# Performance work log

Hardware: AMD Instinct MI355X
Metric: run time of the kernel (lower is better)

Reference implementation:

```python
import jax, jax.numpy as jnp
import numpy as np

H = 1024        # bridge_hidden_dim
NH = 16         # num_attention_heads
HD = H // NH    # head_dim = 64
B, S = 4, 1024
PHYS_W = 0.2
CONS_W = 0.15


def setup_inputs() -> dict:
    key = jax.random.key(0)
    ks = jax.random.split(key, 16)
    sc = 0.02
    return {
        "cnn_features": jax.random.normal(ks[0], (B, S, H), jnp.float32),
        "llm_features": jax.random.normal(ks[1], (B, S, H), jnp.float32),
        "Wq": jax.random.normal(ks[2], (H, H), jnp.float32) * sc,
        "bq": jnp.zeros((H,), jnp.float32),
        "Wk": jax.random.normal(ks[3], (H, H), jnp.float32) * sc,
        "bk": jnp.zeros((H,), jnp.float32),
        "Wv": jax.random.normal(ks[4], (H, H), jnp.float32) * sc,
        "bv": jnp.zeros((H,), jnp.float32),
        "Wo": jax.random.normal(ks[5], (H, H), jnp.float32) * sc,
        "bo": jnp.zeros((H,), jnp.float32),
        "ln_g": jnp.ones((H,), jnp.float32),
        "ln_b": jnp.zeros((H,), jnp.float32),
        "e_energy": jax.random.normal(ks[6], (H,), jnp.float32),
        "e_mass": jax.random.normal(ks[7], (H,), jnp.float32),
        "e_momentum": jax.random.normal(ks[8], (H,), jnp.float32),
    }


def _layernorm(x, g, b, eps=1e-5):
    mu = jnp.mean(x, axis=-1, keepdims=True)
    var = jnp.var(x, axis=-1, keepdims=True)
    return (x - mu) * jax.lax.rsqrt(var + eps) * g + b


def _split_heads(x):
    b, s, _ = x.shape
    return x.reshape(b, s, NH, HD).transpose(0, 2, 1, 3)  # [b, h, s, d]


def _physics_attention(q_in, k_in, v_in, Wq, bq, Wk, bk, Wv, bv, Wo, bo, ln_g, ln_b):
    # q_in: [b, sq, H]; k_in == v_in: [b, sk, H] with sq == sk (required by bias math)
    Q = _split_heads(q_in @ Wq.T + bq)  # [b,h,s,d]
    K = _split_heads(k_in @ Wk.T + bk)
    V = _split_heads(v_in @ Wv.T + bv)
    scores = jnp.einsum('bhqd,bhkd->bhqk', Q, K) / jnp.sqrt(jnp.float32(HD))
    # physics constraints (broadcast [b,h,s,1] over key axis)
    energy_bias = jnp.sum(Q * K, axis=-1, keepdims=True) * PHYS_W
    mass_bias = jnp.mean(Q + K, axis=-1, keepdims=True) * CONS_W
    scores = scores + energy_bias + mass_bias
    attn = jax.nn.softmax(scores, axis=-1)  # dropout is identity in eval
    att = jnp.einsum('bhqk,bhkd->bhqd', attn, V)
    b, h, s, d = att.shape
    att = att.transpose(0, 2, 1, 3).reshape(b, s, h * d)
    out = att @ Wo.T + bo
    return _layernorm(q_in + out, ln_g, ln_b)


def reference(cnn_features, llm_features, Wq, bq, Wk, bk, Wv, bv, Wo, bo,
              ln_g, ln_b, e_energy, e_mass, e_momentum):
    b = cnn_features.shape[0]
    phys = jnp.stack([e_energy, e_mass, e_momentum], axis=0)  # [3, H]
    phys = jnp.broadcast_to(phys[None], (b, 3, H))
    aug_cnn = jnp.concatenate([cnn_features, phys], axis=1)  # [b, S+3, H]
    aug_llm = jnp.concatenate([llm_features, phys], axis=1)
    cnn_att = _physics_attention(aug_cnn, aug_llm, aug_llm,
                                 Wq, bq, Wk, bk, Wv, bv, Wo, bo, ln_g, ln_b)
    llm_att = _physics_attention(aug_llm, aug_cnn, aug_cnn,
                                 Wq, bq, Wk, bk, Wv, bv, Wo, bo, ln_g, ln_b)
    cnn_out = cnn_att[:, :cnn_features.shape[1], :]
    llm_out = llm_att[:, :llm_features.shape[1], :]
    return (cnn_out, llm_out)
```

## Files before the change

kernel.cpp:

```cpp
#include <hip/hip_runtime.h>
#include <stdint.h>

#define SA 1027
#define MROWS 8216
#define MPAD 8320
#define SPAD 1088
#define ATTM 8192

typedef __attribute__((ext_vector_type(8))) short short8;
typedef __attribute__((ext_vector_type(4))) float f32x4;
typedef __attribute__((ext_vector_type(2))) unsigned int u32x2;

typedef const __attribute__((address_space(1))) uint8_t* gas1;
typedef __attribute__((address_space(3))) uint8_t* las3;

__device__ __forceinline__ void gload16(const void* g, void* l){
  __builtin_amdgcn_global_load_lds((gas1)g, (las3)l, 16, 0, 0);
}

__device__ __forceinline__ uint16_t f2bf(float f){
  uint32_t x = __builtin_bit_cast(uint32_t, f);
  x = (x + 0x7fffu + ((x >> 16) & 1u)) >> 16;
  return (uint16_t)x;
}
__device__ __forceinline__ float bf2f(uint16_t u){
  uint32_t x = ((uint32_t)u) << 16;
  return __builtin_bit_cast(float, x);
}

__device__ __forceinline__ f32x4 mfma16(short8 a, short8 b, f32x4 c){
  return __builtin_amdgcn_mfma_f32_16x16x32_bf16(a, b, c, 0, 0, 0);
}

#define QSCALE 0.18033688011112042f

__global__ __launch_bounds__(256) void prep_wb(
    const float* __restrict__ Wq, const float* __restrict__ Wk,
    const float* __restrict__ Wv, const float* __restrict__ Wo,
    const float* __restrict__ bq, const float* __restrict__ bk,
    const float* __restrict__ bv, const float* __restrict__ bo,
    uint16_t* __restrict__ W, float* __restrict__ bias){
  const int gid = blockIdx.x*256 + threadIdx.x;
  if (gid < 1048576){
    const int w = gid >> 18;
    const int off = (gid & 262143) << 2;
    const float* src = (w==0) ? Wq : (w==1) ? Wk : (w==2) ? Wv : Wo;
    const float4 v = *(const float4*)(src + off);
    ushort4 u;
    u.x = f2bf(v.x); u.y = f2bf(v.y); u.z = f2bf(v.z); u.w = f2bf(v.w);
    *(ushort4*)(W + ((size_t)w << 20) + off) = u;
  } else if (gid < 1048576 + 1024){
    const int i = (gid - 1048576) << 2;
    const int w = i >> 10;
    const int off = i & 1023;
    const float* src = (w==0) ? bq : (w==1) ? bk : (w==2) ? bv : bo;
    *(float4*)(bias + i) = *(const float4*)(src + off);
  }
}

__global__ __launch_bounds__(256) void prep_X(
    const float* __restrict__ cnn, const float* __restrict__ llm,
    const float* __restrict__ ee, const float* __restrict__ em,
    const float* __restrict__ ep, uint16_t* __restrict__ X){
  const int row = blockIdx.x;
  const int c4 = threadIdx.x << 2;
  float4 v = {0.f,0.f,0.f,0.f};
  if (row < MROWS){
    const int cb = row / SA;
    const int s = row - cb*SA;
    const int c = cb >> 2, b = cb & 3;
    const float* src;
    if (s < 1024) src = (c ? llm : cnn) + ((size_t)(b*1024 + s))*1024 + c4;
    else src = ((s == 1024) ? ee : (s == 1025) ? em : ep) + c4;
    v = *(const float4*)src;
  }
  ushort4 u;
  u.x = f2bf(v.x); u.y = f2bf(v.y); u.z = f2bf(v.z); u.w = f2bf(v.w);
  *(ushort4*)(X + (size_t)row*1024 + c4) = u;
}

__global__ __launch_bounds__(256) void gemm_bt(
    const uint16_t* __restrict__ A, const uint16_t* __restrict__ B,
    const float* __restrict__ bias, uint16_t* __restrict__ C,
    int K, int lda, int ldb, int ldc, float qscale, int qcols){
  __shared__ __align__(16) uint8_t smA[16384];
  __shared__ __align__(16) uint8_t smB[16384];
  const int tid = threadIdx.x;
  const int lane = tid & 63, wid = tid >> 6;
  const int l15 = lane & 15, l4 = lane >> 4;
  const int orig = blockIdx.y * gridDim.x + blockIdx.x;
  const int cpx = (gridDim.x * gridDim.y) >> 3;
  const int swz = (orig & 7) * cpx + (orig >> 3);
  const int bn = swz % gridDim.x;
  const int bm = swz / gridDim.x;
  const int wr = wid >> 1, wc = wid & 1;

  f32x4 acc[4][4];
  #pragma unroll
  for (int i = 0; i < 4; ++i)
    #pragma unroll
    for (int j = 0; j < 4; ++j) acc[i][j] = (f32x4){0.f,0.f,0.f,0.f};

  const int srow = lane >> 3;
  const int schunk = lane & 7;
  const int KT = K >> 6;
  for (int kt = 0; kt < KT; ++kt){
    __syncthreads();
    #pragma unroll
    for (int j = 0; j < 4; ++j){
      const int cj = wid*4 + j;
      const int row = cj*8 + srow;
      const int gch = schunk ^ (row & 7);
      gload16(A + (size_t)(bm*128 + row)*lda + kt*64 + gch*8, smA + cj*1024);
      gload16(B + (size_t)(bn*128 + row)*ldb + kt*64 + gch*8, smB + cj*1024);
    }
    __syncthreads();
    #pragma unroll
    for (int kk = 0; kk < 2; ++kk){
      short8 af[4], bfr[4];
      #pragma unroll
      for (int i = 0; i < 4; ++i){
        const int row = wr*64 + i*16 + l15;
        af[i] = *(const short8*)(smA + ((row*128 + kk*64 + l4*16) ^ ((row & 7) << 4)));
      }
      #pragma unroll
      for (int j = 0; j < 4; ++j){
        const int row = wc*64 + j*16 + l15;
        bfr[j] = *(const short8*)(smB + ((row*128 + kk*64 + l4*16) ^ ((row & 7) << 4)));
      }
      #pragma unroll
      for (int i = 0; i < 4; ++i)
        #pragma unroll
        for (int j = 0; j < 4; ++j)
          acc[i][j] = mfma16(af[i], bfr[j], acc[i][j]);
    }
  }
  #pragma unroll
  for (int j = 0; j < 4; ++j){
    const int n = bn*128 + wc*64 + j*16 + l15;
    const float bb = bias[n];
    const float sc = (n < qcols) ? qscale : 1.0f;
    #pragma unroll
    for (int i = 0; i < 4; ++i){
      const int m0 = bm*128 + wr*64 + i*16 + l4*4;
      #pragma unroll
      for (int r = 0; r < 4; ++r)
        C[(size_t)(m0 + r)*ldc + n] = f2bf((acc[i][j][r] + bb) * sc);
    }
  }
}

__global__ __launch_bounds__(256) void vtrans(
    const uint16_t* __restrict__ Y, uint16_t* __restrict__ Vt){
  __shared__ uint16_t t[64][65];
  const int bid = blockIdx.x;
  const int st = bid % 17, cbh = bid / 17;
  const int s0 = st*64;
  const int tid = threadIdx.x;
  const int a = tid >> 2, g = tid & 3;
  const int cb = cbh >> 4, h = cbh & 15;
  const int s = s0 + a;
  short8 v0 = {0,0,0,0,0,0,0,0}, v1 = {0,0,0,0,0,0,0,0};
  if (s < SA){
    const uint16_t* p = Y + ((size_t)cb*SA + s)*3072 + 2048 + h*64 + g*16;
    v0 = *(const short8*)p;
    v1 = *(const short8*)(p + 8);
  }
  #pragma unroll
  for (int i=0;i<8;i++){ t[a][g*16+i] = (uint16_t)v0[i]; t[a][g*16+8+i] = (uint16_t)v1[i]; }
  __syncthreads();
  short8 w0, w1;
  #pragma unroll
  for (int i=0;i<8;i++){ w0[i] = (short)t[g*16+i][a]; w1[i] = (short)t[g*16+8+i][a]; }
  uint16_t* o = Vt + ((size_t)cbh*64 + a)*SPAD + s0 + g*16;
  *(short8*)o = w0;
  *(short8*)(o + 8) = w1;
}

__global__ __launch_bounds__(256, 4) void attn_k(
    const uint16_t* __restrict__ Y, const uint16_t* __restrict__ Vt,
    uint16_t* __restrict__ att){
  __shared__ __align__(16) uint8_t smK[16384];
  __shared__ __align__(16) uint8_t smV[16384];
  __shared__ __align__(16) uint8_t smP[8192];
  const int tid = threadIdx.x;
  const int lane = tid & 63, wid = tid >> 6;
  const int l15 = lane & 15, l4 = lane >> 4;
  const int i = blockIdx.x;
  const int inst = (i & 7) * 16 + (i >> 6);
  const int qb = (i >> 3) & 7;
  const int h = inst & 15, cb = inst >> 4;
  const size_t yrow0 = (size_t)cb * SA;
  const int q0 = qb * 128 + wid * 32;
  const size_t vbase = (size_t)inst * 64 * SPAD;
  const uint16_t* Yk = Y + yrow0 * 3072 + 1024 + h * 64;

  short8 qf[2][2];
  #pragma unroll
  for (int u = 0; u < 2; ++u){
    const uint16_t* p = Y + (yrow0 + q0 + u*16 + l15) * 3072 + h * 64 + l4 * 8;
    qf[u][0] = *(const short8*)p;
    qf[u][1] = *(const short8*)(p + 32);
  }

  f32x4 o0[4], o1[4];
  float psum0 = 0.f, psum1 = 0.f;
  #pragma unroll
  for (int d = 0; d < 4; ++d){ o0[d] = (f32x4){0,0,0,0}; o1[d] = (f32x4){0,0,0,0}; }

  int koff[2], pwo[4];
  #pragma unroll
  for (int kk = 0; kk < 2; ++kk)
    koff[kk] = (l15*128 + kk*64 + l4*16) ^ ((l15 & 7) << 4);
  #pragma unroll
  for (int nt = 0; nt < 4; ++nt)
    pwo[nt] = (l15*128 + nt*32 + l4*8) ^ ((l15 & 7) << 4);
  uint8_t* const pb = smP + wid * 2048;

  const int srow = lane >> 3, schunk = lane & 7;
  #pragma unroll
  for (int j = 0; j < 2; ++j){
    const int cj = wid*2 + j;
    const int row = cj*8 + srow;
    const int gch = schunk ^ (row & 7);
    gload16(Yk + (size_t)row * 3072 + gch*8, smK + cj*1024);
    gload16(Vt + vbase + (size_t)row * SPAD + gch*8, smV + cj*1024);
  }
  __syncthreads();

  int cur = 0;
  for (int kt = 0; kt < 17; ++kt){
    if (kt < 16){
      const int s1n = (kt + 1) * 64;
      const int nb = (cur ^ 1) * 8192;
      #pragma unroll
      for (int j = 0; j < 2; ++j){
        const int cj = wid*2 + j;
        const int row = cj*8 + srow;
        const int gch = schunk ^ (row & 7);
        gload16(Yk + (size_t)(s1n + row) * 3072 + gch*8, smK + nb + cj*1024);
        gload16(Vt + vbase + (size_t)row * SPAD + s1n + gch*8, smV + nb + cj*1024);
      }
    }
    const uint8_t* bK = smK + cur * 8192;
    const uint8_t* bV = smV + cur * 8192;

    f32x4 sa[4], sb[4];
    #pragma unroll
    for (int nt = 0; nt < 4; ++nt){
      const short8 k0 = *(const short8*)(bK + nt*2048 + koff[0]);
      const short8 k1 = *(const short8*)(bK + nt*2048 + koff[1]);
      sa[nt] = mfma16(k1, qf[0][1], mfma16(k0, qf[0][0], (f32x4){0,0,0,0}));
      sb[nt] = mfma16(k1, qf[1][1], mfma16(k0, qf[1][0], (f32x4){0,0,0,0}));
    }
    if (kt == 16){
      #pragma unroll
      for (int nt = 0; nt < 4; ++nt)
        #pragma unroll
        for (int r = 0; r < 4; ++r){
          if (nt*16 + l4*4 + r >= 3){ sa[nt][r] = -3e38f; sb[nt][r] = -3e38f; }
        }
    }
    #pragma unroll
    for (int nt = 0; nt < 4; ++nt){
      const float p0 = __builtin_amdgcn_exp2f(sa[nt][0]);
      const float p1 = __builtin_amdgcn_exp2f(sa[nt][1]);
      const float p2 = __builtin_amdgcn_exp2f(sa[nt][2]);
      const float p3 = __builtin_amdgcn_exp2f(sa[nt][3]);
      psum0 += (p0 + p1) + (p2 + p3);
      uint32_t w0, w1;
      asm("v_cvt_pk_bf16_f32 %0, %1, %2" : "=v"(w0) : "v"(p0), "v"(p1));
      asm("v_cvt_pk_bf16_f32 %0, %1, %2" : "=v"(w1) : "v"(p2), "v"(p3));
      *(u32x2*)(pb + pwo[nt]) = (u32x2){w0, w1};
    }
    short8 vf[4][2];
    #pragma unroll
    for (int dt = 0; dt < 4; ++dt){
      vf[dt][0] = *(const short8*)(bV + dt*2048 + koff[0]);
      vf[dt][1] = *(const short8*)(bV + dt*2048 + koff[1]);
    }
    #pragma unroll
    for (int kk = 0; kk < 2; ++kk){
      const short8 pf = *(const short8*)(pb + koff[kk]);
      #pragma unroll
      for (int dt = 0; dt < 4; ++dt)
        o0[dt] = mfma16(pf, vf[dt][kk], o0[dt]);
    }
    #pragma unroll
    for (int nt = 0; nt < 4; ++nt){
      const float p0 = __builtin_amdgcn_exp2f(sb[nt][0]);
      const float p1 = __builtin_amdgcn_exp2f(sb[nt][1]);
      const float p2 = __builtin_amdgcn_exp2f(sb[nt][2]);
      const float p3 = __builtin_amdgcn_exp2f(sb[nt][3]);
      psum1 += (p0 + p1) + (p2 + p3);
      uint32_t w0, w1;
      asm("v_cvt_pk_bf16_f32 %0, %1, %2" : "=v"(w0) : "v"(p0), "v"(p1));
      asm("v_cvt_pk_bf16_f32 %0, %1, %2" : "=v"(w1) : "v"(p2), "v"(p3));
      *(u32x2*)(pb + pwo[nt]) = (u32x2){w0, w1};
    }
    #pragma unroll
    for (int kk = 0; kk < 2; ++kk){
      const short8 pf = *(const short8*)(pb + koff[kk]);
      #pragma unroll
      for (int dt = 0; dt < 4; ++dt)
        o1[dt] = mfma16(pf, vf[dt][kk], o1[dt]);
    }
    __syncthreads();
    cur ^= 1;
  }

  psum0 += __shfl_xor(psum0, 16); psum0 += __shfl_xor(psum0, 32);
  psum1 += __shfl_xor(psum1, 16); psum1 += __shfl_xor(psum1, 32);
  const size_t arow0 = (size_t)cb * 1024 + q0;
  #pragma unroll
  for (int r = 0; r < 4; ++r){
    const float inv0 = 1.f / __shfl(psum0, l4*4 + r);
    const float inv1 = 1.f / __shfl(psum1, l4*4 + r);
    #pragma unroll
    for (int dt = 0; dt < 4; ++dt){
      att[(arow0 + l4*4 + r)*1024 + h*64 + dt*16 + l15] = f2bf(o0[dt][r] * inv0);
      att[(arow0 + 16 + l4*4 + r)*1024 + h*64 + dt*16 + l15] = f2bf(o1[dt][r] * inv1);
    }
  }
}

__global__ __launch_bounds__(256) void ln_out(
    const uint16_t* __restrict__ Op, const float* __restrict__ cnn,
    const float* __restrict__ llm, const float* __restrict__ g,
    const float* __restrict__ b, float* __restrict__ out){
  const int row = blockIdx.x;
  const int c = row >> 12, bq = row & 4095;
  const int tid = threadIdx.x;
  const ushort4 u = *(const ushort4*)(Op + (size_t)row*1024 + (tid<<2));
  const float4 rv = *(const float4*)((c ? llm : cnn) + (size_t)bq*1024 + (tid<<2));
  const float x0 = bf2f(u.x) + rv.x;
  const float x1 = bf2f(u.y) + rv.y;
  const float x2 = bf2f(u.z) + rv.z;
  const float x3 = bf2f(u.w) + rv.w;
  float s1 = x0+x1+x2+x3;
  float s2 = x0*x0+x1*x1+x2*x2+x3*x3;
  #pragma unroll
  for (int m=1;m<64;m<<=1){ s1 += __shfl_xor(s1,m); s2 += __shfl_xor(s2,m); }
  __shared__ float r1[4], r2[4];
  const int wid = tid >> 6, lane = tid & 63;
  if (lane == 0){ r1[wid] = s1; r2[wid] = s2; }
  __syncthreads();
  s1 = r1[0]+r1[1]+r1[2]+r1[3];
  s2 = r2[0]+r2[1]+r2[2]+r2[3];
  const float mu = s1 * 0.0009765625f;
  const float var = s2 * 0.0009765625f - mu*mu;
  const float rs = rsqrtf(var + 1e-5f);
  const float4 gv = *(const float4*)(g + (tid<<2));
  const float4 bv = *(const float4*)(b + (tid<<2));
  float4 ov;
  ov.x = (x0 - mu)*rs*gv.x + bv.x;
  ov.y = (x1 - mu)*rs*gv.y + bv.y;
  ov.z = (x2 - mu)*rs*gv.z + bv.z;
  ov.w = (x3 - mu)*rs*gv.w + bv.w;
  *(float4*)(out + ((size_t)c << 22) + (size_t)bq*1024 + (tid<<2)) = ov;
}

extern "C" void kernel_launch(void* const* d_in, const int* in_sizes, int n_in,
                              void* d_out, int out_size, void* d_ws, size_t ws_size,
                              hipStream_t stream){
  const float* cnn = (const float*)d_in[0];
  const float* llm = (const float*)d_in[1];
  const float* Wq  = (const float*)d_in[2];
  const float* bq  = (const float*)d_in[3];
  const float* Wk  = (const float*)d_in[4];
  const float* bk  = (const float*)d_in[5];
  const float* Wv  = (const float*)d_in[6];
  const float* bv  = (const float*)d_in[7];
  const float* Wo  = (const float*)d_in[8];
  const float* bo  = (const float*)d_in[9];
  const float* lng = (const float*)d_in[10];
  const float* lnb = (const float*)d_in[11];
  const float* ee  = (const float*)d_in[12];
  const float* em  = (const float*)d_in[13];
  const float* ep  = (const float*)d_in[14];

  uint8_t* ws = (uint8_t*)d_ws;
  uint16_t* X    = (uint16_t*)(ws + 0);
  uint16_t* W    = (uint16_t*)(ws + 17039360);
  float*    bias = (float*)   (ws + 25427968);
  uint16_t* Y    = (uint16_t*)(ws + 25444352);
  uint16_t* Vt   = (uint16_t*)(ws + 76562432);
  uint16_t* att  = (uint16_t*)(ws + 94388224);
  uint16_t* Op   = X;
  float* out = (float*)d_out;

  prep_wb<<<4100, 256, 0, stream>>>(Wq, Wk, Wv, Wo, bq, bk, bv, bo, W, bias);
  prep_X<<<MPAD, 256, 0, stream>>>(cnn, llm, ee, em, ep, X);
  gemm_bt<<<dim3(24, 65), 256, 0, stream>>>(X, W, bias, Y, 1024, 1024, 1024, 3072, QSCALE, 1024);
  vtrans<<<128*17, 256, 0, stream>>>(Y, Vt);
  attn_k<<<1024, 256, 0, stream>>>(Y, Vt, att);
  gemm_bt<<<dim3(8, 64), 256, 0, stream>>>(att, W + 3145728, bias + 3072, Op, 1024, 1024, 1024, 1024, 1.0f, 0);
  ln_out<<<ATTM, 256, 0, stream>>>(Op, cnn, llm, lng, lnb, out);
}
```

Before: 191.2 us.

## Replace 128x128 GEMM with double-buffered 256x256 tile pipelined kernel

Swaps the single-stage 128x128 bf16 MFMA GEMM for a 512-thread kernel using 256x256 output tiles, 128 KB of double-buffered dynamic LDS, and async global-to-LDS prefetch interleaved with MFMA phases, using barriers and priority raising. It also remaps blocks across XCDs and pads the input rows to a multiple of 256. The aim is to hide load latency behind compute and improve operand reuse for the QKV and output projections. The cost is one block per CU and a small grid for the output projection (128 blocks), which may leave CUs idle.

```diff
diff --git a/kernel.cpp b/kernel.cpp
--- a/kernel.cpp
+++ b/kernel.cpp
@@ -3,7 +3,7 @@
 
 #define SA 1027
 #define MROWS 8216
-#define MPAD 8320
+#define MPAD 8448
 #define SPAD 1088
 #define ATTM 8192
 
@@ -79,75 +79,155 @@
   *(ushort4*)(X + (size_t)row*1024 + c4) = u;
 }
 
-__global__ __launch_bounds__(256) void gemm_bt(
+__global__ __launch_bounds__(512) void gemm256k(
     const uint16_t* __restrict__ A, const uint16_t* __restrict__ B,
     const float* __restrict__ bias, uint16_t* __restrict__ C,
-    int K, int lda, int ldb, int ldc, float qscale, int qcols){
-  __shared__ __align__(16) uint8_t smA[16384];
-  __shared__ __align__(16) uint8_t smB[16384];
+    int K, int lda, int ldb, int ldc, int nbn, float qscale, int qcols){
+  extern __shared__ uint8_t lds[];
   const int tid = threadIdx.x;
   const int lane = tid & 63, wid = tid >> 6;
   const int l15 = lane & 15, l4 = lane >> 4;
-  const int orig = blockIdx.y * gridDim.x + blockIdx.x;
-  const int cpx = (gridDim.x * gridDim.y) >> 3;
-  const int swz = (orig & 7) * cpx + (orig >> 3);
-  const int bn = swz % gridDim.x;
-  const int bm = swz / gridDim.x;
-  const int wr = wid >> 1, wc = wid & 1;
-
-  f32x4 acc[4][4];
-  #pragma unroll
-  for (int i = 0; i < 4; ++i)
+  const int wm = wid >> 2, wn = wid & 3;
+  const int nwg = gridDim.x;
+  const int q8 = nwg >> 3, r8 = nwg & 7;
+  const int xcd = blockIdx.x & 7, loc = blockIdx.x >> 3;
+  const int wg = (xcd < r8 ? xcd*(q8+1) : r8*(q8+1) + (xcd-r8)*q8) + loc;
+  const int bm = wg / nbn, bn = wg % nbn;
+
+  const uint16_t* Ag = A + (size_t)bm*256*lda;
+  const uint16_t* Bg = B + (size_t)bn*256*ldb;
+
+  const int srow8 = lane >> 3;
+  const int gch = (lane & 7) ^ srow8;
+  const int c0 = wid*2, c1 = c0 + 1;
+  const size_t ga0 = (size_t)(c0*8 + srow8)*lda + gch*8;
+  const size_t ga1 = (size_t)(c1*8 + srow8)*lda + gch*8;
+  const size_t gb0 = (size_t)(c0*8 + srow8)*ldb + gch*8;
+  const size_t gb1 = (size_t)(c1*8 + srow8)*ldb + gch*8;
+
+#define STG_A(buf, H, kt) do { \
+    gload16(Ag + (size_t)(H)*128*lda + (size_t)(kt)*64 + ga0, lds + (buf)*65536 + (H)*16384 + c0*1024); \
+    gload16(Ag + (size_t)(H)*128*lda + (size_t)(kt)*64 + ga1, lds + (buf)*65536 + (H)*16384 + c1*1024); \
+  } while(0)
+#define STG_B(buf, H, kt) do { \
+    gload16(Bg + (size_t)(H)*128*ldb + (size_t)(kt)*64 + gb0, lds + (buf)*65536 + 32768 + (H)*16384 + c0*1024); \
+    gload16(Bg + (size_t)(H)*128*ldb + (size_t)(kt)*64 + gb1, lds + (buf)*65536 + 32768 + (H)*16384 + c1*1024); \
+  } while(0)
+
+  int koff[2];
+  koff[0] = (l4*16) ^ ((l15 & 7) << 4);
+  koff[1] = (64 + l4*16) ^ ((l15 & 7) << 4);
+  const int arow = (wm*128 + l15) * 128;
+  const int brow = (wn*64 + l15) * 128;
+
+  f32x4 acc[8][4];
+  #pragma unroll
+  for (int i = 0; i < 8; ++i)
     #pragma unroll
     for (int j = 0; j < 4; ++j) acc[i][j] = (f32x4){0.f,0.f,0.f,0.f};
 
-  const int srow = lane >> 3;
-  const int schunk = lane & 7;
-  const int KT = K >> 6;
-  for (int kt = 0; kt < KT; ++kt){
-    __syncthreads();
-    #pragma unroll
-    for (int j = 0; j < 4; ++j){
-      const int cj = wid*4 + j;
-      const int row = cj*8 + srow;
-      const int gch = schunk ^ (row & 7);
-      gload16(A + (size_t)(bm*128 + row)*lda + kt*64 + gch*8, smA + cj*1024);
-      gload16(B + (size_t)(bn*128 + row)*ldb + kt*64 + gch*8, smB + cj*1024);
-    }
-    __syncthreads();
-    #pragma unroll
-    for (int kk = 0; kk < 2; ++kk){
-      short8 af[4], bfr[4];
-      #pragma unroll
-      for (int i = 0; i < 4; ++i){
-        const int row = wr*64 + i*16 + l15;
-        af[i] = *(const short8*)(smA + ((row*128 + kk*64 + l4*16) ^ ((row & 7) << 4)));
-      }
-      #pragma unroll
-      for (int j = 0; j < 4; ++j){
-        const int row = wc*64 + j*16 + l15;
-        bfr[j] = *(const short8*)(smB + ((row*128 + kk*64 + l4*16) ^ ((row & 7) << 4)));
-      }
-      #pragma unroll
-      for (int i = 0; i < 4; ++i)
-        #pragma unroll
-        for (int j = 0; j < 4; ++j)
-          acc[i][j] = mfma16(af[i], bfr[j], acc[i][j]);
-    }
-  }
+  const int NT = K >> 6;
+  STG_A(0,0,0); STG_A(0,1,0); STG_B(0,0,0); STG_B(0,1,0);
+  STG_B(1,0,1); STG_B(1,1,1);
+  asm volatile("s_waitcnt vmcnt(4)" ::: "memory");
+  __builtin_amdgcn_s_barrier();
+
+  for (int s = 0; s < NT; ++s){
+    const int b = s & 1;
+    const uint8_t* La = lds + b*65536;
+    const uint8_t* Lb = La + 32768;
+    const int sn1 = (s+1 < NT) ? s+1 : s;
+    const int sn2 = (s+2 < NT) ? s+2 : s;
+    const int nb = b ^ 1;
+    short8 af[4][2], bf0[2][2], bf1[2][2];
+
+    #pragma unroll
+    for (int i = 0; i < 4; ++i){
+      af[i][0] = *(const short8*)(La + arow + i*2048 + koff[0]);
+      af[i][1] = *(const short8*)(La + arow + i*2048 + koff[1]);
+    }
+    #pragma unroll
+    for (int j = 0; j < 2; ++j){
+      bf0[j][0] = *(const short8*)(Lb + brow + j*2048 + koff[0]);
+      bf0[j][1] = *(const short8*)(Lb + brow + j*2048 + koff[1]);
+    }
+    STG_A(nb, 0, sn1);
+    __builtin_amdgcn_s_barrier();
+    asm volatile("s_waitcnt lgkmcnt(0)" ::: "memory");
+    __builtin_amdgcn_sched_barrier(0);
+    __builtin_amdgcn_s_setprio(1);
+    #pragma unroll
+    for (int i = 0; i < 4; ++i)
+      #pragma unroll
+      for (int j = 0; j < 2; ++j)
+        acc[i][j] = mfma16(af[i][1], bf0[j][1], mfma16(af[i][0], bf0[j][0], acc[i][j]));
+    __builtin_amdgcn_s_setprio(0);
+    __builtin_amdgcn_s_barrier();
+
+    #pragma unroll
+    for (int j = 0; j < 2; ++j){
+      bf1[j][0] = *(const short8*)(Lb + brow + (j+2)*2048 + koff[0]);
+      bf1[j][1] = *(const short8*)(Lb + brow + (j+2)*2048 + koff[1]);
+    }
+    STG_A(nb, 1, sn1);
+    __builtin_amdgcn_s_barrier();
+    asm volatile("s_waitcnt lgkmcnt(0)" ::: "memory");
+    __builtin_amdgcn_sched_barrier(0);
+    __builtin_amdgcn_s_setprio(1);
+    #pragma unroll
+    for (int i = 0; i < 4; ++i)
+      #pragma unroll
+      for (int j = 0; j < 2; ++j)
+        acc[i][j+2] = mfma16(af[i][1], bf1[j][1], mfma16(af[i][0], bf1[j][0], acc[i][j+2]));
+    __builtin_amdgcn_s_setprio(0);
+    __builtin_amdgcn_s_barrier();
+
+    #pragma unroll
+    for (int i = 0; i < 4; ++i){
+      af[i][0] = *(const short8*)(La + 8192 + arow + i*2048 + koff[0]);
+      af[i][1] = *(const short8*)(La + 8192 + arow + i*2048 + koff[1]);
+    }
+    STG_B(b, 0, sn2);
+    __builtin_amdgcn_s_barrier();
+    asm volatile("s_waitcnt lgkmcnt(0)" ::: "memory");
+    __builtin_amdgcn_sched_barrier(0);
+    __builtin_amdgcn_s_setprio(1);
+    #pragma unroll
+    for (int i = 0; i < 4; ++i)
+      #pragma unroll
+      for (int j = 0; j < 2; ++j)
+        acc[i+4][j+2] = mfma16(af[i][1], bf1[j][1], mfma16(af[i][0], bf1[j][0], acc[i+4][j+2]));
+    __builtin_amdgcn_s_setprio(0);
+    __builtin_amdgcn_s_barrier();
+
+    STG_B(b, 1, sn2);
+    __builtin_amdgcn_s_barrier();
+    __builtin_amdgcn_s_setprio(1);
+    #pragma unroll
+    for (int i = 0; i < 4; ++i)
+      #pragma unroll
+      for (int j = 0; j < 2; ++j)
+        acc[i+4][j] = mfma16(af[i][1], bf0[j][1], mfma16(af[i][0], bf0[j][0], acc[i+4][j]));
+    __builtin_amdgcn_s_setprio(0);
+    asm volatile("s_waitcnt vmcnt(4)" ::: "memory");
+    __builtin_amdgcn_s_barrier();
+  }
+
   #pragma unroll
   for (int j = 0; j < 4; ++j){
-    const int n = bn*128 + wc*64 + j*16 + l15;
+    const int n = bn*256 + wn*64 + j*16 + l15;
     const float bb = bias[n];
     const float sc = (n < qcols) ? qscale : 1.0f;
     #pragma unroll
-    for (int i = 0; i < 4; ++i){
-      const int m0 = bm*128 + wr*64 + i*16 + l4*4;
+    for (int i = 0; i < 8; ++i){
+      const size_t m0 = (size_t)bm*256 + wm*128 + i*16 + l4*4;
       #pragma unroll
       for (int r = 0; r < 4; ++r)
-        C[(size_t)(m0 + r)*ldc + n] = f2bf((acc[i][j][r] + bb) * sc);
-    }
-  }
+        C[(m0 + r)*ldc + n] = f2bf((acc[i][j][r] + bb) * sc);
+    }
+  }
+#undef STG_A
+#undef STG_B
 }
 
 __global__ __launch_bounds__(256) void vtrans(
@@ -381,19 +461,22 @@
 
   uint8_t* ws = (uint8_t*)d_ws;
   uint16_t* X    = (uint16_t*)(ws + 0);
-  uint16_t* W    = (uint16_t*)(ws + 17039360);
-  float*    bias = (float*)   (ws + 25427968);
-  uint16_t* Y    = (uint16_t*)(ws + 25444352);
-  uint16_t* Vt   = (uint16_t*)(ws + 76562432);
-  uint16_t* att  = (uint16_t*)(ws + 94388224);
-  uint16_t* Op   = X;
+  uint16_t* W    = (uint16_t*)(ws + 17301504);
+  float*    bias = (float*)   (ws + 25690112);
+  uint16_t* Y    = (uint16_t*)(ws + 25706496);
+  uint16_t* Vt   = (uint16_t*)(ws + 77611008);
+  uint16_t* att  = X;
+  uint16_t* Op   = Y;
   float* out = (float*)d_out;
+
+  hipFuncSetAttribute((const void*)gemm256k,
+                      hipFuncAttributeMaxDynamicSharedMemorySize, 131072);
 
   prep_wb<<<4100, 256, 0, stream>>>(Wq, Wk, Wv, Wo, bq, bk, bv, bo, W, bias);
   prep_X<<<MPAD, 256, 0, stream>>>(cnn, llm, ee, em, ep, X);
-  gemm_bt<<<dim3(24, 65), 256, 0, stream>>>(X, W, bias, Y, 1024, 1024, 1024, 3072, QSCALE, 1024);
+  gemm256k<<<396, 512, 131072, stream>>>(X, W, bias, Y, 1024, 1024, 1024, 3072, 12, QSCALE, 1024);
   vtrans<<<128*17, 256, 0, stream>>>(Y, Vt);
   attn_k<<<1024, 256, 0, stream>>>(Y, Vt, att);
-  gemm_bt<<<dim3(8, 64), 256, 0, stream>>>(att, W + 3145728, bias + 3072, Op, 1024, 1024, 1024, 1024, 1.0f, 0);
+  gemm256k<<<128, 512, 131072, stream>>>(att, W + 3145728, bias + 3072, Op, 1024, 1024, 1024, 1024, 4, 1.0f, 0);
   ln_out<<<ATTM, 256, 0, stream>>>(Op, cnn, llm, lng, lnb, out);
 }
```

Result: faster. 184.1 us (-3.7%).
